# Performance work log

Measured on AMD Instinct MI355X. Metric: run time of the kernel, lower is better.

Reference implementation:

```python
import jax, jax.numpy as jnp
import numpy as np

N_EXPERTS = 64
TOPK = 4
DIM = 2048
B_T = 8192


def setup_inputs() -> dict:
    key = jax.random.key(0)
    k1, k2 = jax.random.split(key)
    x = jax.random.normal(k1, (B_T, DIM), jnp.float32)
    W = jax.random.normal(k2, (N_EXPERTS, DIM), jnp.float32) * 0.02  # nn.Linear weight (out, in)
    router_bias = jnp.zeros((N_EXPERTS,), jnp.float32)  # registered buffer, init zeros
    return {"x": x, "W": W, "router_bias": router_bias, "token_capacity": 3072}


def _route(x, W, router_bias, token_capacity):
    """Faithful serial greedy capacity-aware routing.

    Replicates the torch nested loop (k-major, token-minor order):
      - per step, pick argmax over the token's (mutated) logits among experts
        with remaining capacity;
      - full experts whose logit exceeds the chosen one get permanently set
        to -inf in that token's logit row (exactly what the inner while-style
        loop does);
      - if no expert has capacity, selected stays -1, weight 0, and the whole
        row becomes -inf (torch sets the top expert to -inf n_experts times).
    """
    logits0 = x @ W.T + router_bias                       # (N, E)
    scores = jax.nn.softmax(logits0, axis=-1)             # (N, E)
    cap = token_capacity // TOPK                          # python int
    remaining0 = jnp.full((N_EXPERTS,), float(cap), jnp.float32)
    N = x.shape[0]
    NEG = jnp.float32(-jnp.inf)

    def step(carry, i):
        logits, remaining = carry
        b = i % N                                         # token index (k-major order)
        row = logits[b]                                   # (E,)
        masked = jnp.where(remaining > 0, row, NEG)
        chosen = jnp.argmax(masked)
        ok = remaining[chosen] > 0                        # False only if all experts full
        sel = jnp.where(ok, chosen, -1).astype(jnp.int32)
        w = jnp.where(ok, scores[b, chosen], jnp.float32(0.0))
        full = remaining <= 0
        cval = row[chosen]
        # full experts 'above' the chosen one were visited and zapped to -inf
        new_row = jnp.where(ok,
                            jnp.where(full & (row > cval), NEG, row),
                            jnp.full_like(row, NEG))
        logits = logits.at[b].set(new_row)
        remaining = remaining.at[chosen].add(jnp.where(ok, jnp.float32(-1.0), jnp.float32(0.0)))
        return (logits, remaining), (sel, w)

    (_, _), (sel_f, w_f) = jax.lax.scan(step, (logits0, remaining0),
                                        jnp.arange(TOPK * N))
    selected = sel_f.reshape(TOPK, N).T                   # (N, TOPK)
    weights = w_f.reshape(TOPK, N).T                      # (N, TOPK)
    weights = weights / (weights.sum(axis=-1, keepdims=True) + 1e-8)
    return selected, weights


def reference(x, W, router_bias, token_capacity):
    return _route(x, W, router_bias, token_capacity)
```

## Files before the change

### kernel.cpp

```cpp
#include <hip/hip_runtime.h>
#include <math.h>

#define N_TOK 8192
#define DIM   2048
#define NE    64
#define TOPK  4
#define THETA 2e-3f
#define TPB2  16
#define NBLK  (N_TOK / TPB2)

typedef short bf16x8 __attribute__((ext_vector_type(8)));
typedef float f32x4  __attribute__((ext_vector_type(4)));

#define OFF_LOGITS 0
#define OFF_MAXV   (OFF_LOGITS + N_TOK * NE)
#define OFF_DENOM  (OFF_MAXV + N_TOK)
#define OFF_W1     (OFF_DENOM + N_TOK)
#define OFF_C1     (OFF_W1 + N_TOK)
#define OFF_NFLAG  (OFF_C1 + N_TOK)
#define OFF_FLAGL  (OFF_NFLAG + 64)
#define OFF_WH     (OFF_FLAGL + N_TOK)
#define OFF_WL     (OFF_WH + NE * DIM / 2)
#define OFF_WT     (OFF_WL + NE * DIM / 2)
#define OFF_WTMP   (OFF_WT + NE * DIM)

__device__ inline void cvt2(float a, float b, unsigned& hi, unsigned& lo) {
    const unsigned ua = __float_as_uint(a), ub = __float_as_uint(b);
    hi = __builtin_amdgcn_perm(ub, ua, 0x07060302u);
    const float ra = a - __uint_as_float(ua & 0xFFFF0000u);
    const float rb = b - __uint_as_float(ub & 0xFFFF0000u);
    lo = __builtin_amdgcn_perm(__float_as_uint(rb), __float_as_uint(ra), 0x07060302u);
}

union FragU { unsigned u[4]; bf16x8 v; uint4 q; };

__device__ inline void make_frags(const float4& p, const float4& q,
                                  bf16x8& hi, bf16x8& lo) {
    FragU H, L;
    cvt2(p.x, p.y, H.u[0], L.u[0]);
    cvt2(p.z, p.w, H.u[1], L.u[1]);
    cvt2(q.x, q.y, H.u[2], L.u[2]);
    cvt2(q.z, q.w, H.u[3], L.u[3]);
    hi = H.v; lo = L.v;
}

__global__ __launch_bounds__(256)
void k_wc(const float* __restrict__ W, unsigned short* __restrict__ wh,
          unsigned short* __restrict__ wl, float* __restrict__ wt,
          int* __restrict__ nflag) {
    if (blockIdx.x == 0 && threadIdx.x == 0) nflag[0] = 0;
    const int i = (blockIdx.x * 256 + threadIdx.x) * 8;
    const int e = i >> 11, k = i & (DIM - 1);
    const float4 p = *reinterpret_cast<const float4*>(W + i);
    const float4 q = *reinterpret_cast<const float4*>(W + i + 4);
    FragU H, L;
    cvt2(p.x, p.y, H.u[0], L.u[0]);
    cvt2(p.z, p.w, H.u[1], L.u[1]);
    cvt2(q.x, q.y, H.u[2], L.u[2]);
    cvt2(q.z, q.w, H.u[3], L.u[3]);
    *reinterpret_cast<uint4*>(wh + i) = H.q;
    *reinterpret_cast<uint4*>(wl + i) = L.q;
    wt[(size_t)(k + 0) * NE + e] = p.x;
    wt[(size_t)(k + 1) * NE + e] = p.y;
    wt[(size_t)(k + 2) * NE + e] = p.z;
    wt[(size_t)(k + 3) * NE + e] = p.w;
    wt[(size_t)(k + 4) * NE + e] = q.x;
    wt[(size_t)(k + 5) * NE + e] = q.y;
    wt[(size_t)(k + 6) * NE + e] = q.z;
    wt[(size_t)(k + 7) * NE + e] = q.w;
}

__global__ __launch_bounds__(512, 4)
void k_main(const float* __restrict__ x, const unsigned short* __restrict__ wh,
            const unsigned short* __restrict__ wl, const float* __restrict__ bias,
            float* __restrict__ logits, float* __restrict__ maxv,
            float* __restrict__ denomv, float* __restrict__ w1f,
            int* __restrict__ c1, int* __restrict__ nflag, int* __restrict__ flagl) {
    __shared__ float red[8][TPB2][68];
    __shared__ float lbuf[TPB2][68];

    const int tid = threadIdx.x;
    const int w   = tid >> 6;
    const int l   = tid & 63;
    const int t0  = blockIdx.x * TPB2;
    const int m   = l & 15;
    const int g   = l >> 4;
    const int kb  = w * (DIM / 8);

    const float* xp = x + (size_t)(t0 + m) * DIM + kb + g * 8;
    const unsigned short* whp = wh + (size_t)m * DIM + kb + g * 8;
    const unsigned short* wlp = wl + (size_t)m * DIM + kb + g * 8;

    f32x4 accA[4], accB[4];
    #pragma unroll
    for (int nt = 0; nt < 4; ++nt)
        #pragma unroll
        for (int r = 0; r < 4; ++r) { accA[nt][r] = 0.0f; accB[nt][r] = 0.0f; }

    float4 P[2], Q[2];
    uint4  BH[2][4];
    P[0] = *reinterpret_cast<const float4*>(xp);
    Q[0] = *reinterpret_cast<const float4*>(xp + 4);
    #pragma unroll
    for (int nt = 0; nt < 4; ++nt)
        BH[0][nt] = *reinterpret_cast<const uint4*>(whp + (size_t)nt * 16 * DIM);

    #pragma unroll
    for (int step = 0; step < 8; ++step) {
        const int cur = step & 1, nxt = cur ^ 1;
        if (step < 7) {
            P[nxt] = *reinterpret_cast<const float4*>(xp + (step + 1) * 32);
            Q[nxt] = *reinterpret_cast<const float4*>(xp + (step + 1) * 32 + 4);
            #pragma unroll
            for (int nt = 0; nt < 4; ++nt)
                BH[nxt][nt] = *reinterpret_cast<const uint4*>(
                    whp + (size_t)nt * 16 * DIM + (step + 1) * 32);
        }
        uint4 BL[4];
        #pragma unroll
        for (int nt = 0; nt < 4; ++nt)
            BL[nt] = *reinterpret_cast<const uint4*>(
                wlp + (size_t)nt * 16 * DIM + step * 32);

        bf16x8 ah, al;
        make_frags(P[cur], Q[cur], ah, al);

        #pragma unroll
        for (int nt = 0; nt < 4; ++nt) {
            FragU bh; bh.q = BH[cur][nt];
            accA[nt] = __builtin_amdgcn_mfma_f32_16x16x32_bf16(ah, bh.v, accA[nt], 0, 0, 0);
            accB[nt] = __builtin_amdgcn_mfma_f32_16x16x32_bf16(al, bh.v, accB[nt], 0, 0, 0);
        }
        #pragma unroll
        for (int nt = 0; nt < 4; ++nt) {
            FragU bl; bl.q = BL[nt];
            accB[nt] = __builtin_amdgcn_mfma_f32_16x16x32_bf16(ah, bl.v, accB[nt], 0, 0, 0);
        }
    }

    #pragma unroll
    for (int nt = 0; nt < 4; ++nt)
        #pragma unroll
        for (int r = 0; r < 4; ++r)
            red[w][g * 4 + r][nt * 16 + m] = accA[nt][r] + accB[nt][r];
    __syncthreads();

    for (int e2 = tid; e2 < TPB2 * NE; e2 += 512) {
        const int t = e2 >> 6, e = e2 & 63;
        float s = red[0][t][e];
        #pragma unroll
        for (int ww = 1; ww < 8; ++ww) s += red[ww][t][e];
        s += bias[e];
        logits[(size_t)(t0 + t) * NE + e] = s;
        lbuf[t][e] = s;
    }
    __syncthreads();

    #pragma unroll
    for (int tt = 0; tt < 2; ++tt) {
        const int t = w * 2 + tt;
        const float lv = lbuf[t][l];
        float v1 = lv; int i1 = l; float v2 = -INFINITY;
        #pragma unroll
        for (int off = 32; off; off >>= 1) {
            const float ov1 = __shfl_xor(v1, off);
            const int   oi1 = __shfl_xor(i1, off);
            const float ov2 = __shfl_xor(v2, off);
            if (ov1 > v1 || (ov1 == v1 && oi1 < i1)) {
                v2 = fmaxf(v1, ov2); v1 = ov1; i1 = oi1;
            } else {
                v2 = fmaxf(v2, ov1);
            }
        }
        float s = expf(lv - v1);
        #pragma unroll
        for (int off = 32; off; off >>= 1) s += __shfl_xor(s, off);
        if (l == 0) {
            const int row = t0 + t;
            maxv[row]   = v1;
            denomv[row] = s;
            c1[row]     = i1;
            w1f[row]    = 1.0f / s;
            if (v1 - v2 < THETA) {
                const int ix = atomicAdd(nflag, 1);
                flagl[ix] = row;
            }
        }
    }
}

__global__ __launch_bounds__(256)
void k_exact(const int* __restrict__ nflag, const int* __restrict__ flagl,
             const float* __restrict__ x, const float* __restrict__ wt,
             const float* __restrict__ bias, float* __restrict__ logits,
             float* __restrict__ maxv, float* __restrict__ denomv,
             float* __restrict__ w1f, int* __restrict__ c1) {
    __shared__ float part[4][68];
    const int n   = nflag[0];
    const int tid = threadIdx.x;
    const int w   = tid >> 6, l = tid & 63;
    for (int i = blockIdx.x; i < n; i += 128) {
        const int t = flagl[i];
        const float* xr = x + (size_t)t * DIM + w * 512;
        const float* wb = wt + (size_t)(w * 512) * NE + l;
        float a = 0.0f;
        for (int k = 0; k < 512; k += 4) {
            const float4 xv = *reinterpret_cast<const float4*>(xr + k);
            a = fmaf(xv.x, wb[(size_t)(k + 0) * NE], a);
            a = fmaf(xv.y, wb[(size_t)(k + 1) * NE], a);
            a = fmaf(xv.z, wb[(size_t)(k + 2) * NE], a);
            a = fmaf(xv.w, wb[(size_t)(k + 3) * NE], a);
        }
        part[w][l] = a;
        __syncthreads();
        if (w == 0) {
            float lg = bias[l];
            #pragma unroll
            for (int s = 0; s < 4; ++s) lg += part[s][l];
            logits[(size_t)t * NE + l] = lg;
            float v = lg; int idx = l;
            #pragma unroll
            for (int off = 32; off; off >>= 1) {
                const float ov = __shfl_xor(v, off);
                const int   oi = __shfl_xor(idx, off);
                if (ov > v || (ov == v && oi < idx)) { v = ov; idx = oi; }
            }
            float p = expf(lg - v);
            #pragma unroll
            for (int off = 32; off; off >>= 1) p += __shfl_xor(p, off);
            if (l == 0) {
                maxv[t]   = v;
                denomv[t] = p;
                c1[t]     = idx;
                w1f[t]    = 1.0f / p;
            }
        }
        __syncthreads();
    }
}

__global__ __launch_bounds__(256)
void k_decide(const int* __restrict__ c1, const float* __restrict__ w1,
              const float* __restrict__ logits, const float* __restrict__ maxv,
              const float* __restrict__ denomv, const int* __restrict__ tc,
              float* __restrict__ out, float* __restrict__ wtmp) {
    __shared__ int hist[NE];
    __shared__ int flagS;
    const int tid = threadIdx.x;
    if (tid < NE) hist[tid] = 0;
    __syncthreads();
    for (int i = tid; i < N_TOK; i += 256) atomicAdd(&hist[c1[i]], 1);
    __syncthreads();
    const int cap = tc[0] / TOPK;
    if (tid < NE) {
        const bool bad = (TOPK * hist[tid] > cap);
        const unsigned long long mm = __ballot(bad);
        if (tid == 0) flagS = (mm == 0ull) ? 1 : 0;
    }
    __syncthreads();

    if (flagS) {
        const int b = blockIdx.x * 256 + tid;
        const float se = (float)c1[b];
        const float wv = w1[b];
        const float wn = wv / (4.0f * wv + 1e-8f);
        *reinterpret_cast<float4*>(out + (size_t)b * 4) = make_float4(se, se, se, se);
        *reinterpret_cast<float4*>(out + (size_t)N_TOK * TOPK + (size_t)b * 4) =
            make_float4(wn, wn, wn, wn);
        return;
    }

    if (blockIdx.x != 0) return;
    if (tid < 64) {
        const int e = tid;
        int rem = cap;
        for (int k = 0; k < TOPK; ++k) {
            for (int b = 0; b < N_TOK; ++b) {
                const float lg = logits[(size_t)b * NE + e];
                float v = (rem > 0) ? lg : -INFINITY;
                int idx = e;
                #pragma unroll
                for (int off = 32; off; off >>= 1) {
                    const float ov = __shfl_xor(v, off);
                    const int   oi = __shfl_xor(idx, off);
                    if (ov > v || (ov == v && oi < idx)) { v = ov; idx = oi; }
                }
                const bool ok = (v != -INFINITY);
                if (ok && e == idx) rem -= 1;
                const float lc = __shfl(lg, idx);
                if (e == 0) {
                    out[(size_t)b * TOPK + k]  = ok ? (float)idx : -1.0f;
                    wtmp[(size_t)b * TOPK + k] = ok ? expf(lc - maxv[b]) / denomv[b] : 0.0f;
                }
            }
        }
    }
    __syncthreads();
    for (int b = tid; b < N_TOK; b += 256) {
        const float w0 = wtmp[b * 4 + 0], w1_ = wtmp[b * 4 + 1];
        const float w2 = wtmp[b * 4 + 2], w3 = wtmp[b * 4 + 3];
        const float s = ((w0 + w1_) + w2) + w3 + 1e-8f;
        out[N_TOK * TOPK + b * 4 + 0] = w0 / s;
        out[N_TOK * TOPK + b * 4 + 1] = w1_ / s;
        out[N_TOK * TOPK + b * 4 + 2] = w2 / s;
        out[N_TOK * TOPK + b * 4 + 3] = w3 / s;
    }
}

extern "C" void kernel_launch(void* const* d_in, const int* in_sizes, int n_in,
                              void* d_out, int out_size, void* d_ws, size_t ws_size,
                              hipStream_t stream) {
    const float* x    = (const float*)d_in[0];
    const float* W    = (const float*)d_in[1];
    const float* bias = (const float*)d_in[2];
    const int*   tc   = (const int*)d_in[3];

    float* ws       = (float*)d_ws;
    float* logits   = ws + OFF_LOGITS;
    float* maxv     = ws + OFF_MAXV;
    float* denomv   = ws + OFF_DENOM;
    float* w1f      = ws + OFF_W1;
    int*   c1       = (int*)(ws + OFF_C1);
    int*   nflag    = (int*)(ws + OFF_NFLAG);
    int*   flagl    = (int*)(ws + OFF_FLAGL);
    unsigned short* wh = (unsigned short*)(ws + OFF_WH);
    unsigned short* wl = (unsigned short*)(ws + OFF_WL);
    float* wt       = ws + OFF_WT;
    float* wtmp     = ws + OFF_WTMP;
    float* out      = (float*)d_out;

    k_wc<<<NE * DIM / 8 / 256, 256, 0, stream>>>(W, wh, wl, wt, nflag);
    k_main<<<NBLK, 512, 0, stream>>>(x, wh, wl, bias, logits, maxv, denomv,
                                     w1f, c1, nflag, flagl);
    k_exact<<<128, 256, 0, stream>>>(nflag, flagl, x, wt, bias, logits,
                                     maxv, denomv, w1f, c1);
    k_decide<<<N_TOK / 256, 256, 0, stream>>>(c1, w1f, logits, maxv, denomv,
                                              tc, out, wtmp);
}
```

Baseline: 155.0 us.

## Stage x through LDS with coalesced row loads and pre-swizzle W fragments

The main GEMM kernel now loads x rows with fully coalesced float4 loads into a double-buffered padded LDS tile, then reads MFMA A-fragments from LDS, instead of strided per-lane global loads. The weight conversion kernel writes hi/lo bf16 weights in a fragment-ordered layout so each wave reads contiguous 16-byte chunks, and low-part weights are now prefetched alongside high parts. The exact-recompute kernel grid is halved. This adds a barrier per k-window and extra LDS use, which may reduce occupancy.

```diff
diff --git a/kernel.cpp b/kernel.cpp
--- a/kernel.cpp
+++ b/kernel.cpp
@@ -8,6 +8,7 @@
 #define THETA 2e-3f
 #define TPB2  16
 #define NBLK  (N_TOK / TPB2)
+#define RSTR  260
 
 typedef short bf16x8 __attribute__((ext_vector_type(8)));
 typedef float f32x4  __attribute__((ext_vector_type(4)));
@@ -45,37 +46,46 @@
 }
 
 __global__ __launch_bounds__(256)
-void k_wc(const float* __restrict__ W, unsigned short* __restrict__ wh,
-          unsigned short* __restrict__ wl, float* __restrict__ wt,
+void k_wc(const float* __restrict__ W, unsigned short* __restrict__ wh2,
+          unsigned short* __restrict__ wl2, float* __restrict__ wt,
           int* __restrict__ nflag) {
-    if (blockIdx.x == 0 && threadIdx.x == 0) nflag[0] = 0;
-    const int i = (blockIdx.x * 256 + threadIdx.x) * 8;
-    const int e = i >> 11, k = i & (DIM - 1);
-    const float4 p = *reinterpret_cast<const float4*>(W + i);
-    const float4 q = *reinterpret_cast<const float4*>(W + i + 4);
+    const int t = blockIdx.x * 256 + threadIdx.x;
+    if (t == 0) nflag[0] = 0;
+    const int l  = t & 63;
+    const int grp = t >> 6;
+    const int nt = grp & 3;
+    const int kc = grp >> 2;
+    const int e  = nt * 16 + (l & 15);
+    const int k0 = kc * 32 + (l >> 4) * 8;
+
+    const float4 p = *reinterpret_cast<const float4*>(W + (size_t)e * DIM + k0);
+    const float4 q = *reinterpret_cast<const float4*>(W + (size_t)e * DIM + k0 + 4);
     FragU H, L;
     cvt2(p.x, p.y, H.u[0], L.u[0]);
     cvt2(p.z, p.w, H.u[1], L.u[1]);
     cvt2(q.x, q.y, H.u[2], L.u[2]);
     cvt2(q.z, q.w, H.u[3], L.u[3]);
-    *reinterpret_cast<uint4*>(wh + i) = H.q;
-    *reinterpret_cast<uint4*>(wl + i) = L.q;
-    wt[(size_t)(k + 0) * NE + e] = p.x;
-    wt[(size_t)(k + 1) * NE + e] = p.y;
-    wt[(size_t)(k + 2) * NE + e] = p.z;
-    wt[(size_t)(k + 3) * NE + e] = p.w;
-    wt[(size_t)(k + 4) * NE + e] = q.x;
-    wt[(size_t)(k + 5) * NE + e] = q.y;
-    wt[(size_t)(k + 6) * NE + e] = q.z;
-    wt[(size_t)(k + 7) * NE + e] = q.w;
+    const size_t off = (size_t)grp * 512 + l * 8;
+    *reinterpret_cast<uint4*>(wh2 + off) = H.q;
+    *reinterpret_cast<uint4*>(wl2 + off) = L.q;
+
+    wt[(size_t)(k0 + 0) * NE + e] = p.x;
+    wt[(size_t)(k0 + 1) * NE + e] = p.y;
+    wt[(size_t)(k0 + 2) * NE + e] = p.z;
+    wt[(size_t)(k0 + 3) * NE + e] = p.w;
+    wt[(size_t)(k0 + 4) * NE + e] = q.x;
+    wt[(size_t)(k0 + 5) * NE + e] = q.y;
+    wt[(size_t)(k0 + 6) * NE + e] = q.z;
+    wt[(size_t)(k0 + 7) * NE + e] = q.w;
 }
 
 __global__ __launch_bounds__(512, 4)
-void k_main(const float* __restrict__ x, const unsigned short* __restrict__ wh,
-            const unsigned short* __restrict__ wl, const float* __restrict__ bias,
+void k_main(const float* __restrict__ x, const unsigned short* __restrict__ wh2,
+            const unsigned short* __restrict__ wl2, const float* __restrict__ bias,
             float* __restrict__ logits, float* __restrict__ maxv,
             float* __restrict__ denomv, float* __restrict__ w1f,
             int* __restrict__ c1, int* __restrict__ nflag, int* __restrict__ flagl) {
+    __shared__ __align__(16) float xs[2][TPB2 * RSTR];
     __shared__ float red[8][TPB2][68];
     __shared__ float lbuf[TPB2][68];
 
@@ -85,11 +95,15 @@
     const int t0  = blockIdx.x * TPB2;
     const int m   = l & 15;
     const int g   = l >> 4;
-    const int kb  = w * (DIM / 8);
-
-    const float* xp = x + (size_t)(t0 + m) * DIM + kb + g * 8;
-    const unsigned short* whp = wh + (size_t)m * DIM + kb + g * 8;
-    const unsigned short* wlp = wl + (size_t)m * DIM + kb + g * 8;
+
+    const float* xrow0 = x + (size_t)(t0 + 2 * w) * DIM + l * 4;
+    const float* xrow1 = x + (size_t)(t0 + 2 * w + 1) * DIM + l * 4;
+    float* st0 = &xs[0][(2 * w) * RSTR + l * 4];
+    float* st1 = &xs[0][(2 * w + 1) * RSTR + l * 4];
+    const int xs1off = TPB2 * RSTR;
+
+    const unsigned short* bh = wh2 + (size_t)w * 2048 + l * 8;
+    const unsigned short* bl = wl2 + (size_t)w * 2048 + l * 8;
 
     f32x4 accA[4], accB[4];
     #pragma unroll
@@ -97,45 +111,60 @@
         #pragma unroll
         for (int r = 0; r < 4; ++r) { accA[nt][r] = 0.0f; accB[nt][r] = 0.0f; }
 
-    float4 P[2], Q[2];
-    uint4  BH[2][4];
-    P[0] = *reinterpret_cast<const float4*>(xp);
-    Q[0] = *reinterpret_cast<const float4*>(xp + 4);
-    #pragma unroll
-    for (int nt = 0; nt < 4; ++nt)
-        BH[0][nt] = *reinterpret_cast<const uint4*>(whp + (size_t)nt * 16 * DIM);
-
-    #pragma unroll
-    for (int step = 0; step < 8; ++step) {
-        const int cur = step & 1, nxt = cur ^ 1;
-        if (step < 7) {
-            P[nxt] = *reinterpret_cast<const float4*>(xp + (step + 1) * 32);
-            Q[nxt] = *reinterpret_cast<const float4*>(xp + (step + 1) * 32 + 4);
+    {
+        const float4 r0 = *reinterpret_cast<const float4*>(xrow0);
+        const float4 r1 = *reinterpret_cast<const float4*>(xrow1);
+        *reinterpret_cast<float4*>(st0) = r0;
+        *reinterpret_cast<float4*>(st1) = r1;
+    }
+    uint4 BH[2][4], BL[2][4];
+    #pragma unroll
+    for (int nt = 0; nt < 4; ++nt) {
+        BH[0][nt] = *reinterpret_cast<const uint4*>(bh + nt * 512);
+        BL[0][nt] = *reinterpret_cast<const uint4*>(bl + nt * 512);
+    }
+    __syncthreads();
+
+    const int aoff = m * RSTR + w * 32 + g * 8;
+
+    #pragma unroll
+    for (int win = 0; win < 8; ++win) {
+        const int cur = win & 1, nxt = cur ^ 1;
+        float4 nx0, nx1;
+        if (win < 7) {
+            nx0 = *reinterpret_cast<const float4*>(xrow0 + (win + 1) * 256);
+            nx1 = *reinterpret_cast<const float4*>(xrow1 + (win + 1) * 256);
             #pragma unroll
-            for (int nt = 0; nt < 4; ++nt)
+            for (int nt = 0; nt < 4; ++nt) {
                 BH[nxt][nt] = *reinterpret_cast<const uint4*>(
-                    whp + (size_t)nt * 16 * DIM + (step + 1) * 32);
-        }
-        uint4 BL[4];
-        #pragma unroll
-        for (int nt = 0; nt < 4; ++nt)
-            BL[nt] = *reinterpret_cast<const uint4*>(
-                wlp + (size_t)nt * 16 * DIM + step * 32);
-
+                    bh + (size_t)(win + 1) * 16384 + nt * 512);
+                BL[nxt][nt] = *reinterpret_cast<const uint4*>(
+                    bl + (size_t)(win + 1) * 16384 + nt * 512);
+            }
+        }
+
+        const float4 p = *reinterpret_cast<const float4*>(&xs[0][cur * xs1off + aoff]);
+        const float4 q = *reinterpret_cast<const float4*>(&xs[0][cur * xs1off + aoff + 4]);
         bf16x8 ah, al;
-        make_frags(P[cur], Q[cur], ah, al);
+        make_frags(p, q, ah, al);
 
         #pragma unroll
         for (int nt = 0; nt < 4; ++nt) {
-            FragU bh; bh.q = BH[cur][nt];
-            accA[nt] = __builtin_amdgcn_mfma_f32_16x16x32_bf16(ah, bh.v, accA[nt], 0, 0, 0);
-            accB[nt] = __builtin_amdgcn_mfma_f32_16x16x32_bf16(al, bh.v, accB[nt], 0, 0, 0);
+            FragU b; b.q = BH[cur][nt];
+            accA[nt] = __builtin_amdgcn_mfma_f32_16x16x32_bf16(ah, b.v, accA[nt], 0, 0, 0);
+            accB[nt] = __builtin_amdgcn_mfma_f32_16x16x32_bf16(al, b.v, accB[nt], 0, 0, 0);
         }
         #pragma unroll
         for (int nt = 0; nt < 4; ++nt) {
-            FragU bl; bl.q = BL[nt];
-            accB[nt] = __builtin_amdgcn_mfma_f32_16x16x32_bf16(ah, bl.v, accB[nt], 0, 0, 0);
-        }
+            FragU b; b.q = BL[cur][nt];
+            accB[nt] = __builtin_amdgcn_mfma_f32_16x16x32_bf16(ah, b.v, accB[nt], 0, 0, 0);
+        }
+
+        if (win < 7) {
+            *reinterpret_cast<float4*>(st0 + nxt * xs1off) = nx0;
+            *reinterpret_cast<float4*>(st1 + nxt * xs1off) = nx1;
+        }
+        __syncthreads();
     }
 
     #pragma unroll
@@ -199,7 +228,7 @@
     const int n   = nflag[0];
     const int tid = threadIdx.x;
     const int w   = tid >> 6, l = tid & 63;
-    for (int i = blockIdx.x; i < n; i += 128) {
+    for (int i = blockIdx.x; i < n; i += 64) {
         const int t = flagl[i];
         const float* xr = x + (size_t)t * DIM + w * 512;
         const float* wb = wt + (size_t)(w * 512) * NE + l;
@@ -323,17 +352,17 @@
     int*   c1       = (int*)(ws + OFF_C1);
     int*   nflag    = (int*)(ws + OFF_NFLAG);
     int*   flagl    = (int*)(ws + OFF_FLAGL);
-    unsigned short* wh = (unsigned short*)(ws + OFF_WH);
-    unsigned short* wl = (unsigned short*)(ws + OFF_WL);
+    unsigned short* wh2 = (unsigned short*)(ws + OFF_WH);
+    unsigned short* wl2 = (unsigned short*)(ws + OFF_WL);
     float* wt       = ws + OFF_WT;
     float* wtmp     = ws + OFF_WTMP;
     float* out      = (float*)d_out;
 
-    k_wc<<<NE * DIM / 8 / 256, 256, 0, stream>>>(W, wh, wl, wt, nflag);
-    k_main<<<NBLK, 512, 0, stream>>>(x, wh, wl, bias, logits, maxv, denomv,
+    k_wc<<<NE * DIM / 8 / 256, 256, 0, stream>>>(W, wh2, wl2, wt, nflag);
+    k_main<<<NBLK, 512, 0, stream>>>(x, wh2, wl2, bias, logits, maxv, denomv,
                                      w1f, c1, nflag, flagl);
-    k_exact<<<128, 256, 0, stream>>>(nflag, flagl, x, wt, bias, logits,
-                                     maxv, denomv, w1f, c1);
+    k_exact<<<64, 256, 0, stream>>>(nflag, flagl, x, wt, bias, logits,
+                                    maxv, denomv, w1f, c1);
     k_decide<<<N_TOK / 256, 256, 0, stream>>>(c1, w1f, logits, maxv, denomv,
                                               tc, out, wtmp);
 }
```

Result: faster. 131.8 us (-15.0%).
